# Kernel tuning notes

Measured on AMD Instinct MI355X. Metric: run time of the kernel, lower is better.

The kernel has to match this reference:

```python
import jax, jax.numpy as jnp
import numpy as np

EPS = 1e-12
LN_EPS = 1e-5
RIDGE = 0.01
M, L, T = 256, 4096, 2048


def setup_inputs() -> dict:
    key = jax.random.key(0)
    ks = jax.random.split(key, 16)
    inp = {
        "gamma": jax.random.uniform(ks[0], (L,), dtype=jnp.float32),
        "A_re": jax.random.normal(ks[1], (M, L), dtype=jnp.float32),
        "A_im": jax.random.normal(ks[2], (M, L), dtype=jnp.float32),
        "X_re": jax.random.normal(ks[3], (M, T), dtype=jnp.float32),
        "X_im": jax.random.normal(ks[4], (M, T), dtype=jnp.float32),
        # LayerNorm(L) params
        "ln_w": jnp.ones((L,), jnp.float32),
        "ln_b": jnp.zeros((L,), jnp.float32),
        # MultiheadAttention(embed_dim=1, num_heads=1): in_proj [3,1]->[3], out_proj [1,1]->[1]
        "in_w": jax.random.normal(ks[5], (3,), dtype=jnp.float32),
        "in_b": jnp.zeros((3,), jnp.float32),
        "out_w": jax.random.normal(ks[6], (1,), dtype=jnp.float32),
        "out_b": jnp.zeros((1,), jnp.float32),
        # gate Linear(L, L)
        "gate_W": jax.random.normal(ks[7], (L, L), dtype=jnp.float32) * (1.0 / np.sqrt(L)),
        "gate_b": jnp.zeros((L,), jnp.float32),
        # learned scalars
        "delta": jnp.float32(0.5),
        "lmbda": jnp.float32(0.01),
    }
    return inp


def _iaa_forward(gamma, A_re, A_im, X_re, X_im, ln_w, ln_b, in_w, in_b,
                 out_w, out_b, gate_W, gate_b, delta, lmbda):
    A = (A_re + 1j * A_im).astype(jnp.complex64)      # [M, L]
    X = (X_re + 1j * X_im).astype(jnp.complex64)      # [M, T]
    p = gamma                                         # [L]

    # R = A diag(p) A^H + ridge * I   (MxM)
    AP = A * p[None, :].astype(A.dtype)
    R = AP @ A.conj().T + RIDGE * jnp.eye(M, dtype=A.dtype)
    Rinv = jnp.linalg.inv(R)                          # [M, M]

    Ah = A.conj().T                                   # [L, M]
    ARi = Ah @ Rinv                                   # [L, M]
    S = ARi @ X                                       # [L, T]
    q = jnp.sum(jnp.abs(S) ** 2, axis=1)              # [L]
    d = jnp.real(jnp.sum(ARi * Ah, axis=1))           # [L]
    v = q / (d + EPS)

    # constrain_gamma -> sigmoid(delta); use_residual
    dlt = jax.nn.sigmoid(delta)
    u = p + dlt * (v - p)

    # LayerNorm over the full length-L vector
    mu = jnp.mean(u)
    var = jnp.mean((u - mu) ** 2)
    u_p = (u - mu) / jnp.sqrt(var + LN_EPS) * ln_w + ln_b

    # MultiheadAttention(embed_dim=1, num_heads=1) over seq of L tokens, scale = 1/sqrt(1) = 1
    qv = u_p * in_w[0] + in_b[0]                      # [L]
    kv = u_p * in_w[1] + in_b[1]
    vv = u_p * in_w[2] + in_b[2]
    scores = qv[:, None] * kv[None, :]                # [L, L]
    attn = jax.nn.softmax(scores, axis=-1)
    attn_out = (attn @ vv) * out_w[0] + out_b[0]      # [L]

    # gating on u (pre-layernorm), as in the torch code
    g = jax.nn.sigmoid(gate_W @ u + gate_b)           # Linear: u @ W.T + b, u is 1-D -> W @ u + b
    r = g * v + (1.0 - g) * p

    s = r + attn_out
    return jax.nn.relu(s - lmbda)


def reference(gamma, A_re, A_im, X_re, X_im, ln_w, ln_b, in_w, in_b,
              out_w, out_b, gate_W, gate_b, delta, lmbda):
    return _iaa_forward(gamma, A_re, A_im, X_re, X_im, ln_w, ln_b, in_w, in_b,
                        out_w, out_b, gate_W, gate_b, delta, lmbda)
```

## Files before the change

kernel.cpp:

```cpp
#include <hip/hip_runtime.h>
#include <hip/hip_bf16.h>
#include <math.h>

#define MM 256
#define LL 4096
#define TT 2048

typedef __attribute__((ext_vector_type(8))) short bf16x8;
typedef __attribute__((ext_vector_type(4))) float f32x4;
typedef __attribute__((ext_vector_type(4))) unsigned short us4;
typedef unsigned short ushort_t;

#define OFF_G      131072
#define OFF_Q      262144
#define OFF_D      266240
#define OFF_V      270336
#define OFF_U      274432
#define OFF_UP     278528
#define ZERO_FL    290816
#define OFF_RINVP  290816
#define OFF_GP     421888
#define OFF_APL    552960
#define OFF_XPL    2650112
#define OFF_ATP    3698688
#define OFF_WTP    5795840
#define OFF_XA     9990144
#define OFF_XB     10121216
#define OFF_EA     10252288
#define OFF_EB     10383360

#define MFMA3(ACC, AH, AL, BH, BL)                                              \
  ACC = __builtin_amdgcn_mfma_f32_16x16x32_bf16(AH, BH, ACC, 0, 0, 0);          \
  ACC = __builtin_amdgcn_mfma_f32_16x16x32_bf16(AH, BL, ACC, 0, 0, 0);          \
  ACC = __builtin_amdgcn_mfma_f32_16x16x32_bf16(AL, BH, ACC, 0, 0, 0);

__device__ __forceinline__ void split_bf16(float x, ushort_t& h, ushort_t& l) {
  __hip_bfloat16 bh = __float2bfloat16(x);
  h = *(ushort_t*)&bh;
  __hip_bfloat16 bl = __float2bfloat16(x - __bfloat162float(bh));
  l = *(ushort_t*)&bl;
}
__device__ __forceinline__ float bfu2f(ushort_t u) {
  unsigned v = ((unsigned)u) << 16;
  float f;
  __builtin_memcpy(&f, &v, 4);
  return f;
}

__device__ __forceinline__ float wave_red_sum(float v) {
#pragma unroll
  for (int o = 32; o > 0; o >>= 1) v += __shfl_down(v, o);
  return v;
}
__device__ __forceinline__ float wave_red_max(float v) {
#pragma unroll
  for (int o = 32; o > 0; o >>= 1) v = fmaxf(v, __shfl_down(v, o));
  return v;
}
__device__ float blk_red_sum(float v) {
  __shared__ float sh[4];
  int lane = threadIdx.x & 63, wv = threadIdx.x >> 6;
  v = wave_red_sum(v);
  __syncthreads();
  if (lane == 0) sh[wv] = v;
  __syncthreads();
  return sh[0] + sh[1] + sh[2] + sh[3];
}
__device__ float blk_red_max(float v) {
  __shared__ float shm[4];
  int lane = threadIdx.x & 63, wv = threadIdx.x >> 6;
  v = wave_red_max(v);
  __syncthreads();
  if (lane == 0) shm[wv] = v;
  __syncthreads();
  return fmaxf(fmaxf(shm[0], shm[1]), fmaxf(shm[2], shm[3]));
}

__device__ __forceinline__ float2 r_mirror(const float2* __restrict__ R, int i, int j) {
  if ((i >> 6) >= (j >> 6)) return R[i * 256 + j];
  float2 r = R[j * 256 + i];
  r.y = -r.y;
  return r;
}

__global__ __launch_bounds__(256) void k_prep(float* __restrict__ ws,
                                              const float* __restrict__ Are,
                                              const float* __restrict__ Aim,
                                              const float* __restrict__ Xre,
                                              const float* __restrict__ Xim,
                                              const float* __restrict__ gamma) {
  __shared__ float tr[32][33], ti[32][33];
  int bid = blockIdx.x, tid = threadIdx.x;
  if (bid < 1136) {
    int idx = bid * 256 + tid;
    float v = 0.0f;
    if (idx < 131072 && (idx % 514) == 0) v = 0.01f;
    ws[idx] = v;
  } else if (bid < 2160) {
    int i4 = (bid - 1136) * 256 + tid;
    ushort_t* dst = (ushort_t*)(ws + OFF_APL);
    float4 re = ((const float4*)Are)[i4];
    float4 im = ((const float4*)Aim)[i4];
    float4 ga = ((const float4*)gamma)[i4 & (LL / 4 - 1)];
    float sr[4] = {re.x * sqrtf(ga.x), re.y * sqrtf(ga.y), re.z * sqrtf(ga.z), re.w * sqrtf(ga.w)};
    float si[4] = {im.x * sqrtf(ga.x), im.y * sqrtf(ga.y), im.z * sqrtf(ga.z), im.w * sqrtf(ga.w)};
    us4 hr, lr, hi, li;
#pragma unroll
    for (int e = 0; e < 4; ++e) {
      ushort_t h, l;
      split_bf16(sr[e], h, l); hr[e] = h; lr[e] = l;
      split_bf16(si[e], h, l); hi[e] = h; li[e] = l;
    }
    size_t o = (size_t)i4 * 4;
    *(us4*)(dst + o) = hr;
    *(us4*)(dst + (size_t)MM * LL + o) = lr;
    *(us4*)(dst + 2 * (size_t)MM * LL + o) = hi;
    *(us4*)(dst + 3 * (size_t)MM * LL + o) = li;
  } else if (bid < 2672) {
    int i4 = (bid - 2160) * 256 + tid;
    ushort_t* dst = (ushort_t*)(ws + OFF_XPL);
    float4 re = ((const float4*)Xre)[i4];
    float4 im = ((const float4*)Xim)[i4];
    float fr[4] = {re.x, re.y, re.z, re.w};
    float fi[4] = {im.x, im.y, im.z, im.w};
    us4 hr, lr, hi, li;
#pragma unroll
    for (int e = 0; e < 4; ++e) {
      ushort_t h, l;
      split_bf16(fr[e], h, l); hr[e] = h; lr[e] = l;
      split_bf16(fi[e], h, l); hi[e] = h; li[e] = l;
    }
    size_t o = (size_t)i4 * 4;
    *(us4*)(dst + o) = hr;
    *(us4*)(dst + (size_t)MM * TT + o) = lr;
    *(us4*)(dst + 2 * (size_t)MM * TT + o) = hi;
    *(us4*)(dst + 3 * (size_t)MM * TT + o) = li;
  } else {
    int b2 = bid - 2672;
    ushort_t* dst = (ushort_t*)(ws + OFF_ATP);
    int c0 = (b2 & 127) * 32, r0 = (b2 >> 7) * 32;
    int tx = tid & 31, tg = tid >> 5;
#pragma unroll
    for (int i = 0; i < 4; ++i) {
      int r = tg + 8 * i;
      tr[r][tx] = Are[(size_t)(r0 + r) * LL + c0 + tx];
      ti[r][tx] = Aim[(size_t)(r0 + r) * LL + c0 + tx];
    }
    __syncthreads();
#pragma unroll
    for (int i = 0; i < 4; ++i) {
      int rr = tg + 8 * i;
      size_t o = (size_t)(c0 + rr) * 256 + r0 + tx;
      ushort_t h, l;
      split_bf16(tr[tx][rr], h, l);
      dst[o] = h;
      dst[o + 1048576] = l;
      split_bf16(ti[tx][rr], h, l);
      dst[o + 2097152] = h;
      dst[o + 3145728] = l;
    }
  }
}

__global__ __launch_bounds__(256, 4) void k_gram_both(float* __restrict__ ws) {
  __shared__ __align__(16) ushort_t sA[4][64][40];
  __shared__ __align__(16) ushort_t sB[4][64][40];
  const int ti_lu[10] = {0, 1, 1, 2, 2, 2, 3, 3, 3, 3};
  const int tj_lu[10] = {0, 0, 1, 0, 1, 2, 0, 1, 2, 3};
  int bid = blockIdx.x;
  const ushort_t* pl;
  float* C;
  int K, tile, ksplit;
  size_t PS;
  if (bid < 320) {
    pl = (const ushort_t*)(ws + OFF_APL);
    C = ws;
    K = LL;
    PS = (size_t)MM * LL;
    tile = bid % 10;
    ksplit = bid / 10;
  } else {
    int b2 = bid - 320;
    pl = (const ushort_t*)(ws + OFF_XPL);
    C = ws + OFF_G;
    K = TT;
    PS = (size_t)MM * TT;
    tile = b2 % 10;
    ksplit = b2 / 10;
  }
  int kbeg = ksplit * 128;
  int i0 = ti_lu[tile] * 64, j0 = tj_lu[tile] * 64;
  bool diag = (i0 == j0);
  int tid = threadIdx.x;
  int lane = tid & 63, wv = tid >> 6;
  int srow = tid >> 2, sslot = tid & 3;
  int arow = wv * 16 + (lane & 15);
  int kq = (lane >> 4) * 8;
  f32x4 z = {0.f, 0.f, 0.f, 0.f};
  f32x4 Zrr[4], Zri[4], Zir[4], Zii[4];
#pragma unroll
  for (int s = 0; s < 4; ++s) { Zrr[s] = z; Zri[s] = z; Zir[s] = z; Zii[s] = z; }

  for (int chunk = 0; chunk < 4; ++chunk) {
    int k0 = kbeg + chunk * 32;
    __syncthreads();
#pragma unroll
    for (int p = 0; p < 4; ++p) {
      *(bf16x8*)&sA[p][srow][sslot * 8] =
          *(const bf16x8*)(pl + p * PS + (size_t)(i0 + srow) * K + k0 + sslot * 8);
      if (!diag)
        *(bf16x8*)&sB[p][srow][sslot * 8] =
            *(const bf16x8*)(pl + p * PS + (size_t)(j0 + srow) * K + k0 + sslot * 8);
    }
    __syncthreads();
    bf16x8 arh = *(const bf16x8*)&sA[0][arow][kq];
    bf16x8 arl = *(const bf16x8*)&sA[1][arow][kq];
    bf16x8 aih = *(const bf16x8*)&sA[2][arow][kq];
    bf16x8 ail = *(const bf16x8*)&sA[3][arow][kq];
    ushort_t(*bs)[64][40] = diag ? sA : sB;
#pragma unroll
    for (int s = 0; s < 4; ++s) {
      int brow = s * 16 + (lane & 15);
      bf16x8 brh = *(const bf16x8*)&bs[0][brow][kq];
      bf16x8 brl = *(const bf16x8*)&bs[1][brow][kq];
      bf16x8 bih = *(const bf16x8*)&bs[2][brow][kq];
      bf16x8 bil = *(const bf16x8*)&bs[3][brow][kq];
      MFMA3(Zrr[s], arh, arl, brh, brl);
      MFMA3(Zri[s], arh, arl, bih, bil);
      MFMA3(Zir[s], aih, ail, brh, brl);
      MFMA3(Zii[s], aih, ail, bih, bil);
    }
  }
  int rbase = i0 + wv * 16 + (lane >> 4) * 4;
#pragma unroll
  for (int s = 0; s < 4; ++s) {
    int col = j0 + s * 16 + (lane & 15);
#pragma unroll
    for (int r = 0; r < 4; ++r) {
      float re = Zrr[s][r] + Zii[s][r];
      float im = Zir[s][r] - Zri[s][r];
      float* p = C + ((size_t)(rbase + r) * 256 + col) * 2;
      atomicAdd(p, re);
      atomicAdd(p + 1, im);
    }
  }
}

__global__ __launch_bounds__(256) void k_n1(float* __restrict__ ws) {
  __shared__ float2 As[16][17], Bs[16][17];
  const float2* R = (const float2*)ws;
  int bid = blockIdx.x, tid = threadIdx.x;
  if (bid < 256) {
    float2* E1 = (float2*)(ws + OFF_EA);
    int i0 = (bid >> 4) * 16, j0 = (bid & 15) * 16;
    int tx = tid & 15, ty = tid >> 4;
    int rowA = i0 + ty;
    float DiA = R[rowA * 257].x;
    float accx = 0.f, accy = 0.f;
    for (int k0 = 0; k0 < 256; k0 += 16) {
      __syncthreads();
      {
        int c = k0 + tx;
        float2 r = r_mirror(R, rowA, c);
        float dl = (rowA == c) ? 1.0f : 0.0f;
        As[ty][tx] = make_float2(dl - r.x / DiA, -r.y / DiA);
      }
      {
        int rB = k0 + ty, c = j0 + tx;
        float DiB = R[rB * 257].x;
        float2 r = r_mirror(R, rB, c);
        float dl = (rB == c) ? 1.0f : 0.0f;
        Bs[ty][tx] = make_float2(dl - r.x / DiB, -r.y / DiB);
      }
      __syncthreads();
#pragma unroll
      for (int kk = 0; kk < 16; ++kk) {
        float2 a = As[ty][kk], bb = Bs[kk][tx];
        accx += a.x * bb.x - a.y * bb.y;
        accy += a.x * bb.y + a.y * bb.x;
      }
    }
    E1[rowA * 256 + j0 + tx] = make_float2(accx, accy);
  } else if (bid < 512) {
    float2* X1 = (float2*)(ws + OFF_XA);
    int idx = (bid - 256) * 256 + tid;
    int i = idx >> 8, j = idx & 255;
    float Dii = R[i * 257].x;
    float Djj = R[j * 257].x;
    float2 r = r_mirror(R, i, j);
    float dl = (i == j) ? 1.0f : 0.0f;
    float ex = dl - r.x / Dii;
    float ey = -r.y / Dii;
    X1[idx] = make_float2((dl + ex) / Djj, ey / Djj);
  } else {
    const float2* src = (const float2*)(ws + OFF_G);
    ushort_t* dst = (ushort_t*)(ws + OFF_GP);
    int idx = (bid - 512) * 256 + tid;
    int i = idx >> 8, j = idx & 255;
    float2 v = r_mirror(src, i, j);
    ushort_t h, l;
    split_bf16(v.x, h, l);
    dst[idx] = h;
    dst[idx + 65536] = l;
    split_bf16(v.y, h, l);
    dst[idx + 131072] = h;
    dst[idx + 196608] = l;
  }
}

__global__ __launch_bounds__(256) void k_newt_step(const float2* __restrict__ Xin,
                                                   const float2* __restrict__ Ein,
                                                   float2* __restrict__ Xout,
                                                   float2* __restrict__ Eout, int xblocks) {
  __shared__ float2 As[16][17], Bs[16][17];
  int bid = blockIdx.x;
  bool isX = bid < xblocks;
  int b = isX ? bid : bid - xblocks;
  const float2* Bm = isX ? Xin : Ein;
  int i0 = (b >> 4) * 16, j0 = (b & 15) * 16;
  int tx = threadIdx.x & 15, ty = threadIdx.x >> 4;
  float accx = 0.f, accy = 0.f;
  for (int k0 = 0; k0 < 256; k0 += 16) {
    __syncthreads();
    As[ty][tx] = Ein[(i0 + ty) * 256 + k0 + tx];
    Bs[ty][tx] = Bm[(k0 + ty) * 256 + j0 + tx];
    __syncthreads();
#pragma unroll
    for (int kk = 0; kk < 16; ++kk) {
      float2 a = As[ty][kk], bb = Bs[kk][tx];
      accx += a.x * bb.x - a.y * bb.y;
      accy += a.x * bb.y + a.y * bb.x;
    }
  }
  int idx = (i0 + ty) * 256 + j0 + tx;
  if (isX) {
    float2 x = Xin[idx];
    Xout[idx] = make_float2(x.x + accx, x.y + accy);
  } else {
    Eout[idx] = make_float2(accx, accy);
  }
}

__global__ __launch_bounds__(256) void k_newt_fin(const float2* __restrict__ Xin,
                                                  const float2* __restrict__ Ein,
                                                  ushort_t* __restrict__ dst) {
  __shared__ float2 As[16][17], Bs[16][17];
  int b = blockIdx.x;
  int i0 = (b >> 4) * 16, j0 = (b & 15) * 16;
  int tx = threadIdx.x & 15, ty = threadIdx.x >> 4;
  float accx = 0.f, accy = 0.f;
  for (int k0 = 0; k0 < 256; k0 += 16) {
    __syncthreads();
    As[ty][tx] = Ein[(i0 + ty) * 256 + k0 + tx];
    Bs[ty][tx] = Xin[(k0 + ty) * 256 + j0 + tx];
    __syncthreads();
#pragma unroll
    for (int kk = 0; kk < 16; ++kk) {
      float2 a = As[ty][kk], bb = Bs[kk][tx];
      accx += a.x * bb.x - a.y * bb.y;
      accy += a.x * bb.y + a.y * bb.x;
    }
  }
  int idx = (i0 + ty) * 256 + j0 + tx;
  float2 x = Xin[idx];
  float vx = x.x + accx, vy = x.y + accy;
  ushort_t h, l;
  split_bf16(vx, h, l);
  dst[idx] = h;
  dst[idx + 65536] = l;
  split_bf16(vy, h, l);
  dst[idx + 131072] = h;
  dst[idx + 196608] = l;
}

__global__ __launch_bounds__(256) void k_wide_mfma(const ushort_t* __restrict__ Ap,
                                                   const ushort_t* __restrict__ Bp,
                                                   const float* __restrict__ AuxRe,
                                                   const float* __restrict__ AuxIm,
                                                   ushort_t* __restrict__ WTout,
                                                   float* __restrict__ dq, int mode) {
  __shared__ __align__(16) ushort_t sB[4][64][40];
  const ushort_t* arh_p = Ap;
  const ushort_t* arl_p = Ap + 65536;
  const ushort_t* aih_p = Ap + 131072;
  const ushort_t* ail_p = Ap + 196608;
  const ushort_t* brh_p = Bp;
  const ushort_t* brl_p = Bp + 1048576;
  const ushort_t* bih_p = Bp + 2097152;
  const ushort_t* bil_p = Bp + 3145728;
  int j0 = blockIdx.x * 64;
  int i0 = blockIdx.y * 64;
  int tid = threadIdx.x;
  int lane = tid & 63, wv = tid >> 6;
  int srow = tid >> 2, sslot = tid & 3;
  int m = i0 + wv * 16 + (lane & 15);
  int kq = (lane >> 4) * 8;
  f32x4 z = {0.f, 0.f, 0.f, 0.f};
  f32x4 Zrr[4], Zri[4], Zir[4], Zii[4];
#pragma unroll
  for (int s = 0; s < 4; ++s) { Zrr[s] = z; Zri[s] = z; Zir[s] = z; Zii[s] = z; }
  for (int k0 = 0; k0 < 256; k0 += 32) {
    __syncthreads();
    {
      size_t bo = (size_t)(j0 + srow) * 256 + k0 + sslot * 8;
      *(bf16x8*)&sB[0][srow][sslot * 8] = *(const bf16x8*)(brh_p + bo);
      *(bf16x8*)&sB[1][srow][sslot * 8] = *(const bf16x8*)(brl_p + bo);
      *(bf16x8*)&sB[2][srow][sslot * 8] = *(const bf16x8*)(bih_p + bo);
      *(bf16x8*)&sB[3][srow][sslot * 8] = *(const bf16x8*)(bil_p + bo);
    }
    __syncthreads();
    size_t ao = (size_t)m * 256 + k0 + kq;
    bf16x8 arh = *(const bf16x8*)(arh_p + ao);
    bf16x8 arl = *(const bf16x8*)(arl_p + ao);
    bf16x8 aih = *(const bf16x8*)(aih_p + ao);
    bf16x8 ail = *(const bf16x8*)(ail_p + ao);
#pragma unroll
    for (int s = 0; s < 4; ++s) {
      int brow = s * 16 + (lane & 15);
      bf16x8 brh = *(const bf16x8*)&sB[0][brow][kq];
      bf16x8 brl = *(const bf16x8*)&sB[1][brow][kq];
      bf16x8 bih = *(const bf16x8*)&sB[2][brow][kq];
      bf16x8 bil = *(const bf16x8*)&sB[3][brow][kq];
      MFMA3(Zrr[s], arh, arl, brh, brl);
      MFMA3(Zri[s], arh, arl, bih, bil);
      MFMA3(Zir[s], aih, ail, brh, brl);
      MFMA3(Zii[s], aih, ail, bih, bil);
    }
  }
  int rbase = i0 + wv * 16 + (lane >> 4) * 4;
#pragma unroll
  for (int s = 0; s < 4; ++s) {
    int col = j0 + s * 16 + (lane & 15);
    size_t wo = (size_t)col * 256 + rbase;
    float part = 0.f;
    if (mode == 0) {
      us4 hr, lr, hi, li;
#pragma unroll
      for (int r = 0; r < 4; ++r) {
        float re = Zrr[s][r] - Zii[s][r];
        float im = Zri[s][r] + Zir[s][r];
        ushort_t h, l;
        split_bf16(re, h, l);
        hr[r] = h; lr[r] = l;
        split_bf16(im, h, l);
        hi[r] = h; li[r] = l;
        size_t o = (size_t)(rbase + r) * LL + col;
        part += re * AuxRe[o] - im * AuxIm[o];
      }
      *(us4*)(WTout + wo) = hr;
      *(us4*)(WTout + 1048576 + wo) = lr;
      *(us4*)(WTout + 2097152 + wo) = hi;
      *(us4*)(WTout + 3145728 + wo) = li;
    } else {
      us4 wh = *(const us4*)(brh_p + wo);
      us4 wl = *(const us4*)(brl_p + wo);
      us4 wih = *(const us4*)(bih_p + wo);
      us4 wil = *(const us4*)(bil_p + wo);
#pragma unroll
      for (int r = 0; r < 4; ++r) {
        float re = Zrr[s][r] - Zii[s][r];
        float im = Zri[s][r] + Zir[s][r];
        float wx = bfu2f(wh[r]) + bfu2f(wl[r]);
        float wy = bfu2f(wih[r]) + bfu2f(wil[r]);
        part += wx * re + wy * im;
      }
    }
    part += __shfl_down(part, 32);
    part += __shfl_down(part, 16);
    if ((lane >> 4) == 0) atomicAdd(dq + col, part);
  }
}

__global__ __launch_bounds__(256) void k_uvln(float* __restrict__ ws,
                                              const float* __restrict__ gamma,
                                              const float* __restrict__ delta,
                                              const float* __restrict__ lnw,
                                              const float* __restrict__ lnb) {
  const float* q = ws + OFF_Q;
  const float* d = ws + OFF_D;
  float* vvec = ws + OFF_V;
  float* uvec = ws + OFF_U;
  float* up = ws + OFF_UP;
  int tid = threadIdx.x;
  float dlt = 1.0f / (1.0f + expf(-delta[0]));
  float s = 0.f;
  for (int i = tid; i < LL; i += 256) {
    float v = q[i] / (d[i] + 1e-12f);
    float p = gamma[i];
    float u = p + dlt * (v - p);
    vvec[i] = v;
    uvec[i] = u;
    s += u;
  }
  float mu = blk_red_sum(s) * (1.0f / LL);
  float s2 = 0.f;
  for (int i = tid; i < LL; i += 256) { float dd = uvec[i] - mu; s2 += dd * dd; }
  float var = blk_red_sum(s2) * (1.0f / LL);
  float inv = rsqrtf(var + 1e-5f);
  for (int i = tid; i < LL; i += 256) up[i] = (uvec[i] - mu) * inv * lnw[i] + lnb[i];
}

__global__ __launch_bounds__(256) void k_gateattn(const float* __restrict__ ws,
                                                  const float* __restrict__ Wg,
                                                  const float* __restrict__ gb,
                                                  const float* __restrict__ inw,
                                                  const float* __restrict__ inb,
                                                  const float* __restrict__ outw,
                                                  const float* __restrict__ outb,
                                                  const float* __restrict__ gamma,
                                                  const float* __restrict__ lmbda,
                                                  float* __restrict__ out) {
  const float* uvec = ws + OFF_U;
  const float* up = ws + OFF_UP;
  const float* vvec = ws + OFF_V;
  int i = blockIdx.x, tid = threadIdx.x;
  const float4* wr = (const float4*)(Wg + (size_t)i * LL);
  const float4* u4 = (const float4*)uvec;
  float s = 0.f;
  for (int j = tid; j < LL / 4; j += 256) {
    float4 w = wr[j], x = u4[j];
    s += w.x * x.x + w.y * x.y + w.z * x.z + w.w * x.w;
  }
  float tot = blk_red_sum(s);
  float g = 1.0f / (1.0f + expf(-(tot + gb[i])));
  float qv = up[i] * inw[0] + inb[0];
  float w1 = inw[1], b1 = inb[1], w2 = inw[2], b2 = inb[2];
  const float4* up4 = (const float4*)up;
  float mx = -3.4e38f;
  for (int j = tid; j < LL / 4; j += 256) {
    float4 u = up4[j];
    mx = fmaxf(mx, fmaxf(fmaxf(qv * (u.x * w1 + b1), qv * (u.y * w1 + b1)),
                         fmaxf(qv * (u.z * w1 + b1), qv * (u.w * w1 + b1))));
  }
  mx = blk_red_max(mx);
  float den = 0.f, num = 0.f;
  for (int j = tid; j < LL / 4; j += 256) {
    float4 u = up4[j];
    float e0 = expf(qv * (u.x * w1 + b1) - mx);
    float e1 = expf(qv * (u.y * w1 + b1) - mx);
    float e2 = expf(qv * (u.z * w1 + b1) - mx);
    float e3 = expf(qv * (u.w * w1 + b1) - mx);
    den += e0 + e1 + e2 + e3;
    num += e0 * (u.x * w2 + b2) + e1 * (u.y * w2 + b2) + e2 * (u.z * w2 + b2) + e3 * (u.w * w2 + b2);
  }
  den = blk_red_sum(den);
  num = blk_red_sum(num);
  if (tid == 0) {
    float attn = (num / den) * outw[0] + outb[0];
    float r = g * vvec[i] + (1.0f - g) * gamma[i] + attn - lmbda[0];
    out[i] = fmaxf(r, 0.0f);
  }
}

extern "C" void kernel_launch(void* const* d_in, const int* in_sizes, int n_in,
                              void* d_out, int out_size, void* d_ws, size_t ws_size,
                              hipStream_t stream) {
  const float* gamma = (const float*)d_in[0];
  const float* Are   = (const float*)d_in[1];
  const float* Aim   = (const float*)d_in[2];
  const float* Xre   = (const float*)d_in[3];
  const float* Xim   = (const float*)d_in[4];
  const float* lnw   = (const float*)d_in[5];
  const float* lnb   = (const float*)d_in[6];
  const float* inw   = (const float*)d_in[7];
  const float* inb   = (const float*)d_in[8];
  const float* outw  = (const float*)d_in[9];
  const float* outb  = (const float*)d_in[10];
  const float* gateW = (const float*)d_in[11];
  const float* gateb = (const float*)d_in[12];
  const float* delta = (const float*)d_in[13];
  const float* lmbda = (const float*)d_in[14];
  float* out = (float*)d_out;
  float* ws = (float*)d_ws;

  float2* XA = (float2*)(ws + OFF_XA);
  float2* XB = (float2*)(ws + OFF_XB);
  float2* EA = (float2*)(ws + OFF_EA);
  float2* EB = (float2*)(ws + OFF_EB);
  ushort_t* Rinvp = (ushort_t*)(ws + OFF_RINVP);

  k_prep<<<3696, 256, 0, stream>>>(ws, Are, Aim, Xre, Xim, gamma);
  k_gram_both<<<480, 256, 0, stream>>>(ws);
  k_n1<<<768, 256, 0, stream>>>(ws);
  k_newt_step<<<512, 256, 0, stream>>>(XA, EA, XB, EB, 256);
  k_newt_step<<<512, 256, 0, stream>>>(XB, EB, XA, EA, 256);
  k_newt_step<<<512, 256, 0, stream>>>(XA, EA, XB, EB, 256);
  k_newt_fin<<<256, 256, 0, stream>>>(XB, EB, Rinvp);

  k_wide_mfma<<<dim3(64, 4), 256, 0, stream>>>(Rinvp, (ushort_t*)(ws + OFF_ATP),
                                               Are, Aim, (ushort_t*)(ws + OFF_WTP),
                                               ws + OFF_D, 0);
  k_wide_mfma<<<dim3(64, 4), 256, 0, stream>>>((ushort_t*)(ws + OFF_GP),
                                               (ushort_t*)(ws + OFF_WTP),
                                               nullptr, nullptr, nullptr, ws + OFF_Q, 1);
  k_uvln<<<1, 256, 0, stream>>>(ws, gamma, delta, lnw, lnb);
  k_gateattn<<<LL, 256, 0, stream>>>(ws, gateW, gateb, inw, inb, outw, outb, gamma, lmbda, out);
}
```

Before: 308.9 us.

## Replace atomic split-K Gram accumulation with partial buffers and a reduce kernel

```diff
diff --git a/kernel.cpp b/kernel.cpp
--- a/kernel.cpp
+++ b/kernel.cpp
@@ -11,19 +11,19 @@
 typedef __attribute__((ext_vector_type(4))) unsigned short us4;
 typedef unsigned short ushort_t;
 
-#define OFF_G      131072
 #define OFF_Q      262144
 #define OFF_D      266240
 #define OFF_V      270336
 #define OFF_U      274432
 #define OFF_UP     278528
-#define ZERO_FL    290816
 #define OFF_RINVP  290816
 #define OFF_GP     421888
 #define OFF_APL    552960
 #define OFF_XPL    2650112
 #define OFF_ATP    3698688
 #define OFF_WTP    5795840
+#define OFF_PA     5795840
+#define OFF_PX     8417280
 #define OFF_XA     9990144
 #define OFF_XB     10121216
 #define OFF_EA     10252288
@@ -45,6 +45,12 @@
   float f;
   __builtin_memcpy(&f, &v, 4);
   return f;
+}
+
+__device__ __forceinline__ void tile_ij(int t, int& ti, int& tj) {
+  float f = sqrtf(8.0f * (float)t + 1.0f);
+  ti = (int)((f - 1.0f) * 0.5f + 0.001f);
+  tj = t - ((ti * (ti + 1)) >> 1);
 }
 
 __device__ __forceinline__ float wave_red_sum(float v) {
@@ -91,13 +97,10 @@
                                               const float* __restrict__ gamma) {
   __shared__ float tr[32][33], ti[32][33];
   int bid = blockIdx.x, tid = threadIdx.x;
-  if (bid < 1136) {
-    int idx = bid * 256 + tid;
-    float v = 0.0f;
-    if (idx < 131072 && (idx % 514) == 0) v = 0.01f;
-    ws[idx] = v;
-  } else if (bid < 2160) {
-    int i4 = (bid - 1136) * 256 + tid;
+  if (bid < 8) {
+    ((float4*)(ws + OFF_Q))[bid * 256 + tid] = make_float4(0.f, 0.f, 0.f, 0.f);
+  } else if (bid < 1032) {
+    int i4 = (bid - 8) * 256 + tid;
     ushort_t* dst = (ushort_t*)(ws + OFF_APL);
     float4 re = ((const float4*)Are)[i4];
     float4 im = ((const float4*)Aim)[i4];
@@ -116,8 +119,8 @@
     *(us4*)(dst + (size_t)MM * LL + o) = lr;
     *(us4*)(dst + 2 * (size_t)MM * LL + o) = hi;
     *(us4*)(dst + 3 * (size_t)MM * LL + o) = li;
-  } else if (bid < 2672) {
-    int i4 = (bid - 2160) * 256 + tid;
+  } else if (bid < 1544) {
+    int i4 = (bid - 1032) * 256 + tid;
     ushort_t* dst = (ushort_t*)(ws + OFF_XPL);
     float4 re = ((const float4*)Xre)[i4];
     float4 im = ((const float4*)Xim)[i4];
@@ -136,7 +139,7 @@
     *(us4*)(dst + 2 * (size_t)MM * TT + o) = hi;
     *(us4*)(dst + 3 * (size_t)MM * TT + o) = li;
   } else {
-    int b2 = bid - 2672;
+    int b2 = bid - 1544;
     ushort_t* dst = (ushort_t*)(ws + OFF_ATP);
     int c0 = (b2 & 127) * 32, r0 = (b2 >> 7) * 32;
     int tx = tid & 31, tg = tid >> 5;
@@ -169,12 +172,12 @@
   const int tj_lu[10] = {0, 0, 1, 0, 1, 2, 0, 1, 2, 3};
   int bid = blockIdx.x;
   const ushort_t* pl;
-  float* C;
+  float2* P;
   int K, tile, ksplit;
   size_t PS;
   if (bid < 320) {
     pl = (const ushort_t*)(ws + OFF_APL);
-    C = ws;
+    P = (float2*)(ws + OFF_PA) + (size_t)bid * 4096;
     K = LL;
     PS = (size_t)MM * LL;
     tile = bid % 10;
@@ -182,7 +185,7 @@
   } else {
     int b2 = bid - 320;
     pl = (const ushort_t*)(ws + OFF_XPL);
-    C = ws + OFF_G;
+    P = (float2*)(ws + OFF_PX) + (size_t)b2 * 4096;
     K = TT;
     PS = (size_t)MM * TT;
     tile = b2 % 10;
@@ -231,18 +234,62 @@
       MFMA3(Zii[s], aih, ail, bih, bil);
     }
   }
-  int rbase = i0 + wv * 16 + (lane >> 4) * 4;
+  int lrb = wv * 16 + (lane >> 4) * 4;
 #pragma unroll
   for (int s = 0; s < 4; ++s) {
-    int col = j0 + s * 16 + (lane & 15);
+    int lc = s * 16 + (lane & 15);
 #pragma unroll
     for (int r = 0; r < 4; ++r) {
       float re = Zrr[s][r] + Zii[s][r];
       float im = Zir[s][r] - Zri[s][r];
-      float* p = C + ((size_t)(rbase + r) * 256 + col) * 2;
-      atomicAdd(p, re);
-      atomicAdd(p + 1, im);
-    }
+      P[(lrb + r) * 64 + lc] = make_float2(re, im);
+    }
+  }
+}
+
+__global__ __launch_bounds__(256) void k_reduce(float* __restrict__ ws) {
+  int bid = blockIdx.x, tid = threadIdx.x;
+  if (bid < 160) {
+    const float2* PA = (const float2*)(ws + OFF_PA);
+    float2* R2 = (float2*)ws;
+    int t = bid >> 4;
+    int e = ((bid & 15) << 8) + tid;
+    float sx = 0.f, sy = 0.f;
+#pragma unroll 4
+    for (int k = 0; k < 32; ++k) {
+      float2 p = PA[(size_t)(k * 10 + t) * 4096 + e];
+      sx += p.x; sy += p.y;
+    }
+    int ti, tj;
+    tile_ij(t, ti, tj);
+    int i = ti * 64 + (e >> 6), j = tj * 64 + (e & 63);
+    if (i == j) sx += 0.01f;
+    R2[i * 256 + j] = make_float2(sx, sy);
+  } else {
+    const float2* PX = (const float2*)(ws + OFF_PX);
+    ushort_t* dst = (ushort_t*)(ws + OFF_GP);
+    int idx = (bid - 160) * 256 + tid;
+    int i = idx >> 8, j = idx & 255;
+    int ii = i, jj = j;
+    float sgn = 1.f;
+    if ((i >> 6) < (j >> 6)) { ii = j; jj = i; sgn = -1.f; }
+    int ti = ii >> 6, tj = jj >> 6;
+    int t = ((ti * (ti + 1)) >> 1) + tj;
+    int e = ((ii & 63) << 6) + (jj & 63);
+    float sx = 0.f, sy = 0.f;
+#pragma unroll 4
+    for (int k = 0; k < 16; ++k) {
+      float2 p = PX[(size_t)(k * 10 + t) * 4096 + e];
+      sx += p.x; sy += p.y;
+    }
+    sy *= sgn;
+    ushort_t h, l;
+    split_bf16(sx, h, l);
+    dst[idx] = h;
+    dst[idx + 65536] = l;
+    split_bf16(sy, h, l);
+    dst[idx + 131072] = h;
+    dst[idx + 196608] = l;
   }
 }
 
@@ -281,7 +328,7 @@
       }
     }
     E1[rowA * 256 + j0 + tx] = make_float2(accx, accy);
-  } else if (bid < 512) {
+  } else {
     float2* X1 = (float2*)(ws + OFF_XA);
     int idx = (bid - 256) * 256 + tid;
     int i = idx >> 8, j = idx & 255;
@@ -292,19 +339,6 @@
     float ex = dl - r.x / Dii;
     float ey = -r.y / Dii;
     X1[idx] = make_float2((dl + ex) / Djj, ey / Djj);
-  } else {
-    const float2* src = (const float2*)(ws + OFF_G);
-    ushort_t* dst = (ushort_t*)(ws + OFF_GP);
-    int idx = (bid - 512) * 256 + tid;
-    int i = idx >> 8, j = idx & 255;
-    float2 v = r_mirror(src, i, j);
-    ushort_t h, l;
-    split_bf16(v.x, h, l);
-    dst[idx] = h;
-    dst[idx + 65536] = l;
-    split_bf16(v.y, h, l);
-    dst[idx + 131072] = h;
-    dst[idx + 196608] = l;
   }
 }
 
@@ -379,7 +413,7 @@
                                                    const float* __restrict__ AuxIm,
                                                    ushort_t* __restrict__ WTout,
                                                    float* __restrict__ dq, int mode) {
-  __shared__ __align__(16) ushort_t sB[4][64][40];
+  __shared__ __align__(16) ushort_t sB[4][32][40];
   const ushort_t* arh_p = Ap;
   const ushort_t* arl_p = Ap + 65536;
   const ushort_t* aih_p = Ap + 131072;
@@ -388,25 +422,27 @@
   const ushort_t* brl_p = Bp + 1048576;
   const ushort_t* bih_p = Bp + 2097152;
   const ushort_t* bil_p = Bp + 3145728;
-  int j0 = blockIdx.x * 64;
+  int j0 = blockIdx.x * 32;
   int i0 = blockIdx.y * 64;
   int tid = threadIdx.x;
   int lane = tid & 63, wv = tid >> 6;
-  int srow = tid >> 2, sslot = tid & 3;
+  int spos = tid & 127;
+  int srow = spos >> 2, sslot = spos & 3;
+  int p0 = (tid >> 7) * 2;
+  const ushort_t* bp0 = (p0 == 0) ? brh_p : bih_p;
+  const ushort_t* bp1 = (p0 == 0) ? brl_p : bil_p;
   int m = i0 + wv * 16 + (lane & 15);
   int kq = (lane >> 4) * 8;
   f32x4 z = {0.f, 0.f, 0.f, 0.f};
-  f32x4 Zrr[4], Zri[4], Zir[4], Zii[4];
-#pragma unroll
-  for (int s = 0; s < 4; ++s) { Zrr[s] = z; Zri[s] = z; Zir[s] = z; Zii[s] = z; }
+  f32x4 Zrr[2], Zri[2], Zir[2], Zii[2];
+#pragma unroll
+  for (int s = 0; s < 2; ++s) { Zrr[s] = z; Zri[s] = z; Zir[s] = z; Zii[s] = z; }
   for (int k0 = 0; k0 < 256; k0 += 32) {
     __syncthreads();
     {
       size_t bo = (size_t)(j0 + srow) * 256 + k0 + sslot * 8;
-      *(bf16x8*)&sB[0][srow][sslot * 8] = *(const bf16x8*)(brh_p + bo);
-      *(bf16x8*)&sB[1][srow][sslot * 8] = *(const bf16x8*)(brl_p + bo);
-      *(bf16x8*)&sB[2][srow][sslot * 8] = *(const bf16x8*)(bih_p + bo);
-      *(bf16x8*)&sB[3][srow][sslot * 8] = *(const bf16x8*)(bil_p + bo);
+      *(bf16x8*)&sB[p0][srow][sslot * 8] = *(const bf16x8*)(bp0 + bo);
+      *(bf16x8*)&sB[p0 + 1][srow][sslot * 8] = *(const bf16x8*)(bp1 + bo);
     }
     __syncthreads();
     size_t ao = (size_t)m * 256 + k0 + kq;
@@ -415,7 +451,7 @@
     bf16x8 aih = *(const bf16x8*)(aih_p + ao);
     bf16x8 ail = *(const bf16x8*)(ail_p + ao);
 #pragma unroll
-    for (int s = 0; s < 4; ++s) {
+    for (int s = 0; s < 2; ++s) {
       int brow = s * 16 + (lane & 15);
       bf16x8 brh = *(const bf16x8*)&sB[0][brow][kq];
       bf16x8 brl = *(const bf16x8*)&sB[1][brow][kq];
@@ -429,7 +465,7 @@
   }
   int rbase = i0 + wv * 16 + (lane >> 4) * 4;
 #pragma unroll
-  for (int s = 0; s < 4; ++s) {
+  for (int s = 0; s < 2; ++s) {
     int col = j0 + s * 16 + (lane & 15);
     size_t wo = (size_t)col * 256 + rbase;
     float part = 0.f;
@@ -579,20 +615,21 @@
   float2* EB = (float2*)(ws + OFF_EB);
   ushort_t* Rinvp = (ushort_t*)(ws + OFF_RINVP);
 
-  k_prep<<<3696, 256, 0, stream>>>(ws, Are, Aim, Xre, Xim, gamma);
+  k_prep<<<2568, 256, 0, stream>>>(ws, Are, Aim, Xre, Xim, gamma);
   k_gram_both<<<480, 256, 0, stream>>>(ws);
-  k_n1<<<768, 256, 0, stream>>>(ws);
+  k_reduce<<<416, 256, 0, stream>>>(ws);
+  k_n1<<<512, 256, 0, stream>>>(ws);
   k_newt_step<<<512, 256, 0, stream>>>(XA, EA, XB, EB, 256);
   k_newt_step<<<512, 256, 0, stream>>>(XB, EB, XA, EA, 256);
   k_newt_step<<<512, 256, 0, stream>>>(XA, EA, XB, EB, 256);
   k_newt_fin<<<256, 256, 0, stream>>>(XB, EB, Rinvp);
 
-  k_wide_mfma<<<dim3(64, 4), 256, 0, stream>>>(Rinvp, (ushort_t*)(ws + OFF_ATP),
-                                               Are, Aim, (ushort_t*)(ws + OFF_WTP),
-                                               ws + OFF_D, 0);
-  k_wide_mfma<<<dim3(64, 4), 256, 0, stream>>>((ushort_t*)(ws + OFF_GP),
-                                               (ushort_t*)(ws + OFF_WTP),
-                                               nullptr, nullptr, nullptr, ws + OFF_Q, 1);
+  k_wide_mfma<<<dim3(128, 4), 256, 0, stream>>>(Rinvp, (ushort_t*)(ws + OFF_ATP),
+                                                Are, Aim, (ushort_t*)(ws + OFF_WTP),
+                                                ws + OFF_D, 0);
+  k_wide_mfma<<<dim3(128, 4), 256, 0, stream>>>((ushort_t*)(ws + OFF_GP),
+                                                (ushort_t*)(ws + OFF_WTP),
+                                                nullptr, nullptr, nullptr, ws + OFF_Q, 1);
   k_uvln<<<1, 256, 0, stream>>>(ws, gamma, delta, lnw, lnb);
   k_gateattn<<<LL, 256, 0, stream>>>(ws, gateW, gateb, inw, inb, outw, outb, gamma, lmbda, out);
 }
```

After: 293.8 us. 1.05x faster.
